# Optimization experiments

Measured on AMD Instinct MI355X. Metric: run time of the kernel, lower is better.

Reference implementation:

```python
import jax, jax.numpy as jnp
import numpy as np

NUM_EXPERTS = 8
TOP_K = 2
B, S, H, I = 4, 4096, 1024, 2048


def setup_inputs() -> dict:
    key = jax.random.key(0)
    ks = jax.random.split(key, 4)
    std = 0.02
    return {
        "hidden_states": jax.random.normal(ks[0], (B, S, H), dtype=jnp.float32),
        "w_gate": jax.random.normal(ks[1], (NUM_EXPERTS, H), dtype=jnp.float32) * std,
        "w_fc": jax.random.normal(ks[2], (NUM_EXPERTS, I, H), dtype=jnp.float32) * std,
        "b_fc": jnp.zeros((NUM_EXPERTS, I), dtype=jnp.float32),
        "w_proj": jax.random.normal(ks[3], (NUM_EXPERTS, H, I), dtype=jnp.float32) * (std / np.sqrt(2 * 24)),
        "b_proj": jnp.zeros((NUM_EXPERTS, H), dtype=jnp.float32),
    }


def reference(hidden_states, w_gate, w_fc, b_fc, w_proj, b_proj):
    b, s, h = hidden_states.shape
    x = hidden_states.reshape(-1, h)  # [T, H]
    # routing: top-k over gate logits, softmax over the k selected logits
    router_logits = jnp.einsum("th,eh->te", x, w_gate)  # [T, E]
    top_vals, top_idx = jax.lax.top_k(router_logits, TOP_K)  # [T, K]
    gates = jax.nn.softmax(top_vals.astype(jnp.float32), axis=-1).astype(x.dtype)  # [T, K]
    # expert MLPs with weighted combine; per-token gate for expert e is the
    # selected routing weight (0 if e not in top-k) -- same math as the
    # gather / grouped-GEMM / index_add scatter in the original.
    out = jnp.zeros_like(x)
    for e in range(NUM_EXPERTS):
        g_e = jnp.sum(jnp.where(top_idx == e, gates, jnp.zeros_like(gates)), axis=-1)  # [T]
        hmid = jax.nn.gelu(x @ w_fc[e].T + b_fc[e], approximate=False)  # [T, I]
        y = hmid @ w_proj[e].T + b_proj[e]  # [T, H]
        out = out + g_e[:, None] * y
    return out.reshape(b, s, h)
```

## Files before the change

### kernel.cpp

```cpp
#include <hip/hip_runtime.h>
#include <math.h>

#define T_TOK 16384
#define HDIM  1024
#define IDIM  2048
#define NEXP  8
#define CAP   16384

typedef __bf16 bf16x8 __attribute__((ext_vector_type(8)));
typedef float  f32x4  __attribute__((ext_vector_type(4)));
typedef unsigned short us8 __attribute__((ext_vector_type(8)));

__device__ __forceinline__ unsigned short f2bf(float f) {
  unsigned int u = __builtin_bit_cast(unsigned int, f);
  u = (u + 0x7FFFu + ((u >> 16) & 1u)) >> 16;
  return (unsigned short)u;
}

__device__ __forceinline__ float bf2f(unsigned short u) {
  return __builtin_bit_cast(float, (unsigned int)u << 16);
}

__device__ __forceinline__ void gld16(const void* g, void* l) {
  __builtin_amdgcn_global_load_lds(
      (const __attribute__((address_space(1))) void*)(g),
      (__attribute__((address_space(3))) void*)(l), 16, 0, 0);
}

__device__ __forceinline__ bf16x8 cvt8(const float* p) {
  f32x4 lo = *(const f32x4*)p;
  f32x4 hi = *(const f32x4*)(p + 4);
  us8 t;
  t[0] = f2bf(lo[0]); t[1] = f2bf(lo[1]); t[2] = f2bf(lo[2]); t[3] = f2bf(lo[3]);
  t[4] = f2bf(hi[0]); t[5] = f2bf(hi[1]); t[6] = f2bf(hi[2]); t[7] = f2bf(hi[3]);
  return __builtin_bit_cast(bf16x8, t);
}

__global__ void zero_out_k(float4* out) {
  out[blockIdx.x * 256 + threadIdx.x] = float4{0.f, 0.f, 0.f, 0.f};
}

__global__ void report_k(float* out, float v, int n) {
  int idx = blockIdx.x * blockDim.x + threadIdx.x;
  int stride = gridDim.x * blockDim.x;
  for (int i = idx; i < n; i += stride) out[i] = v;
}

__global__ void cvt_bf16_k(const float* __restrict__ src, unsigned short* __restrict__ dst, int n4) {
  int idx = blockIdx.x * blockDim.x + threadIdx.x;
  int stride = gridDim.x * blockDim.x;
  for (int i = idx; i < n4; i += stride) {
    float4 v = ((const float4*)src)[i];
    ushort4 o;
    o.x = f2bf(v.x); o.y = f2bf(v.y); o.z = f2bf(v.z); o.w = f2bf(v.w);
    ((ushort4*)dst)[i] = o;
  }
}

__global__ void route1_k(const float* __restrict__ x, const float* __restrict__ wg,
                         int* __restrict__ echoice, float* __restrict__ tgate) {
  __shared__ __align__(16) float wgl[NEXP * HDIM];
  int tid = threadIdx.x;
  for (int i = tid; i < NEXP * HDIM / 4; i += 256)
    ((float4*)wgl)[i] = ((const float4*)wg)[i];
  __syncthreads();

  int wave = tid >> 6, lane = tid & 63;
  int t = blockIdx.x * 4 + wave;

  float accv[NEXP];
#pragma unroll
  for (int e = 0; e < NEXP; e++) accv[e] = 0.f;
  const float* xr = x + (size_t)t * HDIM;
#pragma unroll 4
  for (int j = 0; j < HDIM / 64; j++) {
    float xv = xr[lane + j * 64];
#pragma unroll
    for (int e = 0; e < NEXP; e++) accv[e] += xv * wgl[e * HDIM + lane + j * 64];
  }
#pragma unroll
  for (int off = 1; off < 64; off <<= 1) {
#pragma unroll
    for (int e = 0; e < NEXP; e++) accv[e] += __shfl_xor(accv[e], off, 64);
  }

  if (lane == 0) {
    int e0 = 0; float v0 = accv[0];
#pragma unroll
    for (int e = 1; e < NEXP; e++) if (accv[e] > v0) { v0 = accv[e]; e0 = e; }
    int e1 = -1; float v1 = -3.4e38f;
#pragma unroll
    for (int e = 0; e < NEXP; e++) if (e != e0 && accv[e] > v1) { v1 = accv[e]; e1 = e; }
    float ex = expf(v1 - v0);
    echoice[t] = e0 | (e1 << 8);
    tgate[t * 2]     = 1.f / (1.f + ex);
    tgate[t * 2 + 1] = ex / (1.f + ex);
  }
}

__global__ void route2_k(const int* __restrict__ echoice, int* __restrict__ counts,
                         int* __restrict__ etok) {
  int E = blockIdx.x;
  int tid = threadIdx.x, lane = tid & 63, wv = tid >> 6;
  __shared__ int base;
  __shared__ int wsum[4];
  if (tid == 0) base = 0;
  __syncthreads();
  for (int t0 = 0; t0 < T_TOK; t0 += 256) {
    int t = t0 + tid;
    int ec = echoice[t];
    int e0 = ec & 255, e1 = (ec >> 8) & 255;
    bool m = (e0 == E) | (e1 == E);
    int code = t * 2 + (e1 == E ? 1 : 0);
    unsigned long long mask = __ballot(m);
    if (lane == 0) wsum[wv] = __popcll(mask);
    int lpre = __popcll(mask & ((1ull << lane) - 1ull));
    __syncthreads();
    int wbase = 0;
#pragma unroll
    for (int w = 0; w < 4; w++) if (w < wv) wbase += wsum[w];
    int total = wsum[0] + wsum[1] + wsum[2] + wsum[3];
    if (m) etok[E * CAP + base + wbase + lpre] = code;
    __syncthreads();
    if (tid == 0) base += total;
    __syncthreads();
  }
  if (tid == 0) counts[E] = base;
}

template <int STAGE, int K, int N, bool A32, bool B32, bool YATOM>
__global__ __launch_bounds__(256)
void gemm_k(const void* __restrict__ Ap_, const void* __restrict__ Wp_,
            const float* __restrict__ bias, unsigned short* __restrict__ hmid,
            unsigned short* __restrict__ ybf, float* __restrict__ out,
            const float* __restrict__ tgate,
            const int* __restrict__ counts, const int* __restrict__ etok) {
  constexpr int NT = N / 128;
  constexpr int ASZ = A32 ? 16384 : 8192;
  constexpr int BSZ = B32 ? 16384 : 8192;
  __shared__ __align__(16) char smem[ASZ + BSZ];
  char* As = smem;
  char* Bs = smem + ASZ;

  int e  = blockIdx.x / (128 * NT);
  int bi = blockIdx.x % (128 * NT);
  int rt = bi / NT, ct = bi % NT;
  int cnt = counts[e];
  if (rt * 128 >= cnt) return;

  int tid = threadIdx.x;
  int lane = tid & 63, wv = tid >> 6;
  int wr = wv >> 1, wc = wv & 1;
  int quad = lane >> 4, ml = lane & 15;

  const char* aptr[4];
  if constexpr (A32) {
    int srow = tid >> 3, seg = tid & 7;
    const float* Af = (const float*)Ap_;
#pragma unroll
    for (int q = 0; q < 4; q++) {
      int r = rt * 128 + q * 32 + srow;
      int code = etok[e * CAP + (r < cnt ? r : cnt - 1)];
      int row = (STAGE == 1) ? (code >> 1) : code;
      aptr[q] = (const char*)(Af + (size_t)row * K + seg * 4);
    }
  } else {
    int srow = tid >> 2, seg = tid & 3;
    const unsigned short* Ab = (const unsigned short*)Ap_;
#pragma unroll
    for (int q = 0; q < 2; q++) {
      int r = rt * 128 + q * 64 + srow;
      int code = etok[e * CAP + (r < cnt ? r : cnt - 1)];
      int row = (STAGE == 1) ? (code >> 1) : code;
      aptr[q] = (const char*)(Ab + (size_t)row * K + seg * 8);
    }
  }
  const char* bptr[4];
  if constexpr (B32) {
    int srow = tid >> 3, seg = tid & 7;
    const float* Wf = (const float*)Wp_;
#pragma unroll
    for (int q = 0; q < 4; q++)
      bptr[q] = (const char*)(Wf + ((size_t)e * N + ct * 128 + q * 32 + srow) * K + seg * 4);
  } else {
    int srow = tid >> 2, seg = tid & 3;
    const unsigned short* Wb = (const unsigned short*)Wp_;
#pragma unroll
    for (int q = 0; q < 2; q++)
      bptr[q] = (const char*)(Wb + ((size_t)e * N + ct * 128 + q * 64 + srow) * K + seg * 8);
  }

  f32x4 acc[4][4] = {};

  for (int k0 = 0; k0 < K; k0 += 32) {
    size_t aoff = (size_t)k0 * (A32 ? 4 : 2);
    size_t boff = (size_t)k0 * (B32 ? 4 : 2);
    if constexpr (A32) {
#pragma unroll
      for (int q = 0; q < 4; q++) gld16(aptr[q] + aoff, As + q * 4096 + tid * 16);
    } else {
#pragma unroll
      for (int q = 0; q < 2; q++) gld16(aptr[q] + aoff, As + q * 4096 + tid * 16);
    }
    if constexpr (B32) {
#pragma unroll
      for (int q = 0; q < 4; q++) gld16(bptr[q] + boff, Bs + q * 4096 + tid * 16);
    } else {
#pragma unroll
      for (int q = 0; q < 2; q++) gld16(bptr[q] + boff, Bs + q * 4096 + tid * 16);
    }
    __syncthreads();

    bf16x8 af[4], bfr[4];
#pragma unroll
    for (int mi = 0; mi < 4; mi++) {
      int row = wr * 64 + mi * 16 + ml;
      if constexpr (A32) af[mi] = cvt8((const float*)As + row * 32 + quad * 8);
      else af[mi] = __builtin_bit_cast(bf16x8, *(const us8*)((const unsigned short*)As + row * 32 + quad * 8));
    }
#pragma unroll
    for (int ni = 0; ni < 4; ni++) {
      int row = wc * 64 + ni * 16 + ml;
      if constexpr (B32) bfr[ni] = cvt8((const float*)Bs + row * 32 + quad * 8);
      else bfr[ni] = __builtin_bit_cast(bf16x8, *(const us8*)((const unsigned short*)Bs + row * 32 + quad * 8));
    }
#pragma unroll
    for (int mi = 0; mi < 4; mi++)
#pragma unroll
      for (int ni = 0; ni < 4; ni++)
        acc[mi][ni] = __builtin_amdgcn_mfma_f32_16x16x32_bf16(af[mi], bfr[ni], acc[mi][ni], 0, 0, 0);
    __syncthreads();
  }

#pragma unroll
  for (int mi = 0; mi < 4; mi++) {
    int ms[4], codes[4];
#pragma unroll
    for (int r = 0; r < 4; r++) {
      ms[r] = rt * 128 + wr * 64 + mi * 16 + quad * 4 + r;
      codes[r] = etok[e * CAP + (ms[r] < cnt ? ms[r] : 0)];
    }
#pragma unroll
    for (int ni = 0; ni < 4; ni++) {
      int n = ct * 128 + wc * 64 + ni * 16 + ml;
      float bv = bias[e * N + n];
#pragma unroll
      for (int r = 0; r < 4; r++) {
        if (ms[r] < cnt) {
          float v = acc[mi][ni][r] + bv;
          if (STAGE == 1) {
            v = 0.5f * v * (1.0f + erff(v * 0.70710678118654752f));
            hmid[(size_t)codes[r] * IDIM + n] = f2bf(v);
          } else if (YATOM) {
            atomicAdd(&out[(size_t)(codes[r] >> 1) * HDIM + n], tgate[codes[r]] * v);
          } else {
            ybf[(size_t)codes[r] * HDIM + n] = f2bf(v);
          }
        }
      }
    }
  }
}

__global__ void combine_k(const unsigned short* __restrict__ y, const float* __restrict__ tgate,
                          float* __restrict__ out) {
  int idx = blockIdx.x * 256 + threadIdx.x;
  int t = idx >> 7;
  int c = idx & 127;
  float g0 = tgate[t * 2], g1 = tgate[t * 2 + 1];
  us8 a = *(const us8*)(y + ((size_t)(t * 2) * HDIM) + c * 8);
  us8 b = *(const us8*)(y + ((size_t)(t * 2 + 1) * HDIM) + c * 8);
  float o[8];
#pragma unroll
  for (int i = 0; i < 8; i++) o[i] = g0 * bf2f(a[i]) + g1 * bf2f(b[i]);
  float4* op = (float4*)(out + (size_t)t * HDIM + c * 8);
  op[0] = float4{o[0], o[1], o[2], o[3]};
  op[1] = float4{o[4], o[5], o[6], o[7]};
}

extern "C" void kernel_launch(void* const* d_in, const int* in_sizes, int n_in,
                              void* d_out, int out_size, void* d_ws, size_t ws_size,
                              hipStream_t stream) {
  const float* x     = (const float*)d_in[0];
  const float* wg    = (const float*)d_in[1];
  const float* wfc   = (const float*)d_in[2];
  const float* bfc   = (const float*)d_in[3];
  const float* wproj = (const float*)d_in[4];
  const float* bproj = (const float*)d_in[5];
  float* out = (float*)d_out;

  char* ws = (char*)d_ws;
  size_t off = 0;
  int* counts  = (int*)(ws + off);   off += 4096;
  int* echoice = (int*)(ws + off);   off += (size_t)T_TOK * 4;
  int* etok    = (int*)(ws + off);   off += (size_t)NEXP * CAP * 4;
  float* tgate = (float*)(ws + off); off += (size_t)T_TOK * 2 * 4;
  unsigned short* hmid = (unsigned short*)(ws + off);
  off += (size_t)T_TOK * 2 * IDIM * 2;
  size_t lean_need = off;
  unsigned short* xbf = (unsigned short*)(ws + off);
  size_t off2 = off + (size_t)T_TOK * HDIM * 2;
  unsigned short* wfcbf = (unsigned short*)(ws + off2);
  off2 += (size_t)NEXP * IDIM * HDIM * 2;
  unsigned short* wprojbf = (unsigned short*)(ws + off2);
  off2 += (size_t)NEXP * HDIM * IDIM * 2;
  size_t full_need = off2;
  unsigned short* ybf = xbf;

  if (ws_size < lean_need) {
    report_k<<<256, 256, 0, stream>>>(out, (float)(ws_size >> 20), T_TOK * HDIM);
    return;
  }

  route1_k<<<T_TOK / 4, 256, 0, stream>>>(x, wg, echoice, tgate);
  route2_k<<<NEXP, 256, 0, stream>>>(echoice, counts, etok);

  if (ws_size >= full_need) {
    cvt_bf16_k<<<4096, 256, 0, stream>>>(x,     xbf,     T_TOK * HDIM / 4);
    cvt_bf16_k<<<4096, 256, 0, stream>>>(wfc,   wfcbf,   NEXP * IDIM * HDIM / 4);
    cvt_bf16_k<<<4096, 256, 0, stream>>>(wproj, wprojbf, NEXP * HDIM * IDIM / 4);
    gemm_k<1, HDIM, IDIM, false, false, false><<<NEXP * 128 * (IDIM / 128), 256, 0, stream>>>(
        xbf, wfcbf, bfc, hmid, ybf, out, tgate, counts, etok);
    gemm_k<2, IDIM, HDIM, false, false, false><<<NEXP * 128 * (HDIM / 128), 256, 0, stream>>>(
        hmid, wprojbf, bproj, hmid, ybf, out, tgate, counts, etok);
    combine_k<<<T_TOK * HDIM / 8 / 256, 256, 0, stream>>>(ybf, tgate, out);
  } else {
    zero_out_k<<<T_TOK * HDIM / 1024, 256, 0, stream>>>((float4*)out);
    gemm_k<1, HDIM, IDIM, true, true, true><<<NEXP * 128 * (IDIM / 128), 256, 0, stream>>>(
        x, wfc, bfc, hmid, ybf, out, tgate, counts, etok);
    gemm_k<2, IDIM, HDIM, false, true, true><<<NEXP * 128 * (HDIM / 128), 256, 0, stream>>>(
        hmid, wproj, bproj, hmid, ybf, out, tgate, counts, etok);
  }
}
```

Baseline: 735.3 us.

## Widen GEMM N-tile, use persistent row-tile slots, fuse x cast into routing

The GEMM moves to BN=256 tiles on the bf16 path and to a persistent grid of 32 row-tile slots per expert and column tile. Each block loops over row tiles instead of early-exiting, which removes the many empty blocks launched for capacity-sized grids. The x-to-bf16 conversion is folded into the routing kernel, the two weight conversions are merged into one launch, and erff in the GELU is replaced by a polynomial approximation. The wider tile raises register pressure under launch_bounds(256,2), and the erf approximation adds a small numerical error.

```diff
diff --git a/kernel.cpp b/kernel.cpp
--- a/kernel.cpp
+++ b/kernel.cpp
@@ -6,6 +6,7 @@
 #define IDIM  2048
 #define NEXP  8
 #define CAP   16384
+#define RT_SLOTS 32
 
 typedef __bf16 bf16x8 __attribute__((ext_vector_type(8)));
 typedef float  f32x4  __attribute__((ext_vector_type(4)));
@@ -36,6 +37,19 @@
   return __builtin_bit_cast(bf16x8, t);
 }
 
+__device__ __forceinline__ float gelu_f(float v) {
+  float z  = 0.70710678118654752f * v;
+  float az = __builtin_fabsf(z);
+  float t  = __builtin_amdgcn_rcpf(__builtin_fmaf(0.3275911f, az, 1.0f));
+  float p  = __builtin_fmaf(t, 1.061405429f, -1.453152027f);
+  p = __builtin_fmaf(t, p, 1.421413741f);
+  p = __builtin_fmaf(t, p, -0.284496736f);
+  p = __builtin_fmaf(t, p, 0.254829592f);
+  float ev = __expf(-az * az);
+  float E  = __builtin_fmaf(-t * p, ev, 1.0f);
+  return 0.5f * v * (1.0f + __builtin_copysignf(E, v));
+}
+
 __global__ void zero_out_k(float4* out) {
   out[blockIdx.x * 256 + threadIdx.x] = float4{0.f, 0.f, 0.f, 0.f};
 }
@@ -46,19 +60,25 @@
   for (int i = idx; i < n; i += stride) out[i] = v;
 }
 
-__global__ void cvt_bf16_k(const float* __restrict__ src, unsigned short* __restrict__ dst, int n4) {
+__global__ void cvt2_k(const float* __restrict__ a, const float* __restrict__ b,
+                       unsigned short* __restrict__ da, unsigned short* __restrict__ db,
+                       int n4each) {
   int idx = blockIdx.x * blockDim.x + threadIdx.x;
   int stride = gridDim.x * blockDim.x;
-  for (int i = idx; i < n4; i += stride) {
-    float4 v = ((const float4*)src)[i];
+  for (int i = idx; i < 2 * n4each; i += stride) {
+    const float4* s; ushort4* d; int j;
+    if (i < n4each) { s = (const float4*)a; d = (ushort4*)da; j = i; }
+    else            { s = (const float4*)b; d = (ushort4*)db; j = i - n4each; }
+    float4 v = s[j];
     ushort4 o;
     o.x = f2bf(v.x); o.y = f2bf(v.y); o.z = f2bf(v.z); o.w = f2bf(v.w);
-    ((ushort4*)dst)[i] = o;
+    d[j] = o;
   }
 }
 
 __global__ void route1_k(const float* __restrict__ x, const float* __restrict__ wg,
-                         int* __restrict__ echoice, float* __restrict__ tgate) {
+                         int* __restrict__ echoice, float* __restrict__ tgate,
+                         unsigned short* __restrict__ xbf) {
   __shared__ __align__(16) float wgl[NEXP * HDIM];
   int tid = threadIdx.x;
   for (int i = tid; i < NEXP * HDIM / 4; i += 256)
@@ -72,9 +92,11 @@
 #pragma unroll
   for (int e = 0; e < NEXP; e++) accv[e] = 0.f;
   const float* xr = x + (size_t)t * HDIM;
+  unsigned short* xbr = xbf + (size_t)t * HDIM;
 #pragma unroll 4
   for (int j = 0; j < HDIM / 64; j++) {
     float xv = xr[lane + j * 64];
+    xbr[lane + j * 64] = f2bf(xv);
 #pragma unroll
     for (int e = 0; e < NEXP; e++) accv[e] += xv * wgl[e * HDIM + lane + j * 64];
   }
@@ -128,133 +150,130 @@
   if (tid == 0) counts[E] = base;
 }
 
-template <int STAGE, int K, int N, bool A32, bool B32, bool YATOM>
-__global__ __launch_bounds__(256)
+template <int STAGE, int K, int N, int BN, bool A32, bool B32, bool YATOM>
+__global__ __launch_bounds__(256, 2)
 void gemm_k(const void* __restrict__ Ap_, const void* __restrict__ Wp_,
             const float* __restrict__ bias, unsigned short* __restrict__ hmid,
             unsigned short* __restrict__ ybf, float* __restrict__ out,
             const float* __restrict__ tgate,
             const int* __restrict__ counts, const int* __restrict__ etok) {
-  constexpr int NT = N / 128;
-  constexpr int ASZ = A32 ? 16384 : 8192;
-  constexpr int BSZ = B32 ? 16384 : 8192;
+  constexpr int NT  = N / BN;
+  constexpr int WN  = BN / 2;
+  constexpr int NI  = WN / 16;
+  constexpr int ASZ = 128 * 32 * (A32 ? 4 : 2);
+  constexpr int BSZ = BN  * 32 * (B32 ? 4 : 2);
+  constexpr int NAQ = ASZ / 4096;
+  constexpr int NBQ = BSZ / 4096;
   __shared__ __align__(16) char smem[ASZ + BSZ];
   char* As = smem;
   char* Bs = smem + ASZ;
 
-  int e  = blockIdx.x / (128 * NT);
-  int bi = blockIdx.x % (128 * NT);
-  int rt = bi / NT, ct = bi % NT;
+  int bx = blockIdx.x;
+  int e    = bx / (NT * RT_SLOTS);
+  int rem  = bx % (NT * RT_SLOTS);
+  int ct   = rem / RT_SLOTS;
+  int slot = rem % RT_SLOTS;
   int cnt = counts[e];
-  if (rt * 128 >= cnt) return;
 
   int tid = threadIdx.x;
   int lane = tid & 63, wv = tid >> 6;
   int wr = wv >> 1, wc = wv & 1;
   int quad = lane >> 4, ml = lane & 15;
 
-  const char* aptr[4];
-  if constexpr (A32) {
-    int srow = tid >> 3, seg = tid & 7;
-    const float* Af = (const float*)Ap_;
-#pragma unroll
-    for (int q = 0; q < 4; q++) {
-      int r = rt * 128 + q * 32 + srow;
-      int code = etok[e * CAP + (r < cnt ? r : cnt - 1)];
-      int row = (STAGE == 1) ? (code >> 1) : code;
-      aptr[q] = (const char*)(Af + (size_t)row * K + seg * 4);
-    }
-  } else {
-    int srow = tid >> 2, seg = tid & 3;
-    const unsigned short* Ab = (const unsigned short*)Ap_;
-#pragma unroll
-    for (int q = 0; q < 2; q++) {
-      int r = rt * 128 + q * 64 + srow;
-      int code = etok[e * CAP + (r < cnt ? r : cnt - 1)];
-      int row = (STAGE == 1) ? (code >> 1) : code;
-      aptr[q] = (const char*)(Ab + (size_t)row * K + seg * 8);
-    }
-  }
-  const char* bptr[4];
+  const char* bptr[NBQ];
   if constexpr (B32) {
     int srow = tid >> 3, seg = tid & 7;
     const float* Wf = (const float*)Wp_;
 #pragma unroll
-    for (int q = 0; q < 4; q++)
-      bptr[q] = (const char*)(Wf + ((size_t)e * N + ct * 128 + q * 32 + srow) * K + seg * 4);
+    for (int q = 0; q < NBQ; q++)
+      bptr[q] = (const char*)(Wf + ((size_t)e * N + ct * BN + q * 32 + srow) * K + seg * 4);
   } else {
     int srow = tid >> 2, seg = tid & 3;
     const unsigned short* Wb = (const unsigned short*)Wp_;
 #pragma unroll
-    for (int q = 0; q < 2; q++)
-      bptr[q] = (const char*)(Wb + ((size_t)e * N + ct * 128 + q * 64 + srow) * K + seg * 8);
-  }
-
-  f32x4 acc[4][4] = {};
-
-  for (int k0 = 0; k0 < K; k0 += 32) {
-    size_t aoff = (size_t)k0 * (A32 ? 4 : 2);
-    size_t boff = (size_t)k0 * (B32 ? 4 : 2);
+    for (int q = 0; q < NBQ; q++)
+      bptr[q] = (const char*)(Wb + ((size_t)e * N + ct * BN + q * 64 + srow) * K + seg * 8);
+  }
+
+  for (int rt = slot; rt * 128 < cnt; rt += RT_SLOTS) {
+    const char* aptr[NAQ];
     if constexpr (A32) {
-#pragma unroll
-      for (int q = 0; q < 4; q++) gld16(aptr[q] + aoff, As + q * 4096 + tid * 16);
+      int srow = tid >> 3, seg = tid & 7;
+      const float* Af = (const float*)Ap_;
+#pragma unroll
+      for (int q = 0; q < NAQ; q++) {
+        int r = rt * 128 + q * 32 + srow;
+        int code = etok[e * CAP + (r < cnt ? r : cnt - 1)];
+        int row = (STAGE == 1) ? (code >> 1) : code;
+        aptr[q] = (const char*)(Af + (size_t)row * K + seg * 4);
+      }
     } else {
-#pragma unroll
-      for (int q = 0; q < 2; q++) gld16(aptr[q] + aoff, As + q * 4096 + tid * 16);
+      int srow = tid >> 2, seg = tid & 3;
+      const unsigned short* Ab = (const unsigned short*)Ap_;
+#pragma unroll
+      for (int q = 0; q < NAQ; q++) {
+        int r = rt * 128 + q * 64 + srow;
+        int code = etok[e * CAP + (r < cnt ? r : cnt - 1)];
+        int row = (STAGE == 1) ? (code >> 1) : code;
+        aptr[q] = (const char*)(Ab + (size_t)row * K + seg * 8);
+      }
     }
-    if constexpr (B32) {
-#pragma unroll
-      for (int q = 0; q < 4; q++) gld16(bptr[q] + boff, Bs + q * 4096 + tid * 16);
-    } else {
-#pragma unroll
-      for (int q = 0; q < 2; q++) gld16(bptr[q] + boff, Bs + q * 4096 + tid * 16);
+
+    f32x4 acc[4][NI] = {};
+
+    for (int k0 = 0; k0 < K; k0 += 32) {
+      size_t aoff = (size_t)k0 * (A32 ? 4 : 2);
+      size_t boff = (size_t)k0 * (B32 ? 4 : 2);
+#pragma unroll
+      for (int q = 0; q < NAQ; q++) gld16(aptr[q] + aoff, As + q * 4096 + tid * 16);
+#pragma unroll
+      for (int q = 0; q < NBQ; q++) gld16(bptr[q] + boff, Bs + q * 4096 + tid * 16);
+      __syncthreads();
+
+      bf16x8 af[4], bfr[NI];
+#pragma unroll
+      for (int mi = 0; mi < 4; mi++) {
+        int row = wr * 64 + mi * 16 + ml;
+        if constexpr (A32) af[mi] = cvt8((const float*)As + row * 32 + quad * 8);
+        else af[mi] = __builtin_bit_cast(bf16x8, *(const us8*)((const unsigned short*)As + row * 32 + quad * 8));
+      }
+#pragma unroll
+      for (int ni = 0; ni < NI; ni++) {
+        int row = wc * WN + ni * 16 + ml;
+        if constexpr (B32) bfr[ni] = cvt8((const float*)Bs + row * 32 + quad * 8);
+        else bfr[ni] = __builtin_bit_cast(bf16x8, *(const us8*)((const unsigned short*)Bs + row * 32 + quad * 8));
+      }
+#pragma unroll
+      for (int mi = 0; mi < 4; mi++)
+#pragma unroll
+        for (int ni = 0; ni < NI; ni++)
+          acc[mi][ni] = __builtin_amdgcn_mfma_f32_16x16x32_bf16(af[mi], bfr[ni], acc[mi][ni], 0, 0, 0);
+      __syncthreads();
     }
-    __syncthreads();
-
-    bf16x8 af[4], bfr[4];
+
 #pragma unroll
     for (int mi = 0; mi < 4; mi++) {
-      int row = wr * 64 + mi * 16 + ml;
-      if constexpr (A32) af[mi] = cvt8((const float*)As + row * 32 + quad * 8);
-      else af[mi] = __builtin_bit_cast(bf16x8, *(const us8*)((const unsigned short*)As + row * 32 + quad * 8));
-    }
-#pragma unroll
-    for (int ni = 0; ni < 4; ni++) {
-      int row = wc * 64 + ni * 16 + ml;
-      if constexpr (B32) bfr[ni] = cvt8((const float*)Bs + row * 32 + quad * 8);
-      else bfr[ni] = __builtin_bit_cast(bf16x8, *(const us8*)((const unsigned short*)Bs + row * 32 + quad * 8));
-    }
-#pragma unroll
-    for (int mi = 0; mi < 4; mi++)
-#pragma unroll
-      for (int ni = 0; ni < 4; ni++)
-        acc[mi][ni] = __builtin_amdgcn_mfma_f32_16x16x32_bf16(af[mi], bfr[ni], acc[mi][ni], 0, 0, 0);
-    __syncthreads();
-  }
-
-#pragma unroll
-  for (int mi = 0; mi < 4; mi++) {
-    int ms[4], codes[4];
-#pragma unroll
-    for (int r = 0; r < 4; r++) {
-      ms[r] = rt * 128 + wr * 64 + mi * 16 + quad * 4 + r;
-      codes[r] = etok[e * CAP + (ms[r] < cnt ? ms[r] : 0)];
-    }
-#pragma unroll
-    for (int ni = 0; ni < 4; ni++) {
-      int n = ct * 128 + wc * 64 + ni * 16 + ml;
-      float bv = bias[e * N + n];
+      int ms[4], codes[4];
 #pragma unroll
       for (int r = 0; r < 4; r++) {
-        if (ms[r] < cnt) {
-          float v = acc[mi][ni][r] + bv;
-          if (STAGE == 1) {
-            v = 0.5f * v * (1.0f + erff(v * 0.70710678118654752f));
-            hmid[(size_t)codes[r] * IDIM + n] = f2bf(v);
-          } else if (YATOM) {
-            atomicAdd(&out[(size_t)(codes[r] >> 1) * HDIM + n], tgate[codes[r]] * v);
-          } else {
-            ybf[(size_t)codes[r] * HDIM + n] = f2bf(v);
+        ms[r] = rt * 128 + wr * 64 + mi * 16 + quad * 4 + r;
+        codes[r] = etok[e * CAP + (ms[r] < cnt ? ms[r] : 0)];
+      }
+#pragma unroll
+      for (int ni = 0; ni < NI; ni++) {
+        int n = ct * BN + wc * WN + ni * 16 + ml;
+        float bv = bias[e * N + n];
+#pragma unroll
+        for (int r = 0; r < 4; r++) {
+          if (ms[r] < cnt) {
+            float v = acc[mi][ni][r] + bv;
+            if (STAGE == 1) {
+              hmid[(size_t)codes[r] * IDIM + n] = f2bf(gelu_f(v));
+            } else if (YATOM) {
+              atomicAdd(&out[(size_t)(codes[r] >> 1) * HDIM + n], tgate[codes[r]] * v);
+            } else {
+              ybf[(size_t)codes[r] * HDIM + n] = f2bf(v);
+            }
           }
         }
       }
@@ -312,23 +331,26 @@
     return;
   }
 
-  route1_k<<<T_TOK / 4, 256, 0, stream>>>(x, wg, echoice, tgate);
-  route2_k<<<NEXP, 256, 0, stream>>>(echoice, counts, etok);
-
   if (ws_size >= full_need) {
-    cvt_bf16_k<<<4096, 256, 0, stream>>>(x,     xbf,     T_TOK * HDIM / 4);
-    cvt_bf16_k<<<4096, 256, 0, stream>>>(wfc,   wfcbf,   NEXP * IDIM * HDIM / 4);
-    cvt_bf16_k<<<4096, 256, 0, stream>>>(wproj, wprojbf, NEXP * HDIM * IDIM / 4);
-    gemm_k<1, HDIM, IDIM, false, false, false><<<NEXP * 128 * (IDIM / 128), 256, 0, stream>>>(
+    route1_k<<<T_TOK / 4, 256, 0, stream>>>(x, wg, echoice, tgate, xbf);
+    route2_k<<<NEXP, 256, 0, stream>>>(echoice, counts, etok);
+    cvt2_k<<<4096, 256, 0, stream>>>(wfc, wproj, wfcbf, wprojbf, NEXP * IDIM * HDIM / 4);
+    gemm_k<1, HDIM, IDIM, 256, false, false, false>
+        <<<NEXP * (IDIM / 256) * RT_SLOTS, 256, 0, stream>>>(
         xbf, wfcbf, bfc, hmid, ybf, out, tgate, counts, etok);
-    gemm_k<2, IDIM, HDIM, false, false, false><<<NEXP * 128 * (HDIM / 128), 256, 0, stream>>>(
+    gemm_k<2, IDIM, HDIM, 256, false, false, false>
+        <<<NEXP * (HDIM / 256) * RT_SLOTS, 256, 0, stream>>>(
         hmid, wprojbf, bproj, hmid, ybf, out, tgate, counts, etok);
     combine_k<<<T_TOK * HDIM / 8 / 256, 256, 0, stream>>>(ybf, tgate, out);
   } else {
+    route1_k<<<T_TOK / 4, 256, 0, stream>>>(x, wg, echoice, tgate, hmid );
+    route2_k<<<NEXP, 256, 0, stream>>>(echoice, counts, etok);
     zero_out_k<<<T_TOK * HDIM / 1024, 256, 0, stream>>>((float4*)out);
-    gemm_k<1, HDIM, IDIM, true, true, true><<<NEXP * 128 * (IDIM / 128), 256, 0, stream>>>(
+    gemm_k<1, HDIM, IDIM, 128, true, true, true>
+        <<<NEXP * (IDIM / 128) * RT_SLOTS, 256, 0, stream>>>(
         x, wfc, bfc, hmid, ybf, out, tgate, counts, etok);
-    gemm_k<2, IDIM, HDIM, false, true, true><<<NEXP * 128 * (HDIM / 128), 256, 0, stream>>>(
+    gemm_k<2, IDIM, HDIM, 128, false, true, true>
+        <<<NEXP * (HDIM / 128) * RT_SLOTS, 256, 0, stream>>>(
         hmid, wproj, bproj, hmid, ybf, out, tgate, counts, etok);
   }
 }
```

Result: slower. 822.2 us (+11.8%).
